# Optimization experiments

Hardware: AMD Instinct MI355X
Metric: run time of the kernel (lower is better)

The kernel has to match this reference:

```python
import jax, jax.numpy as jnp
import numpy as np

BN_EPS = 1e-5

def _haar_details(x):
    # pywt.dwt2(x, 'haar') details for even H, W.
    # Block [[p, q], [r, s]] with p = x[2i,2j], q = x[2i,2j+1], r = x[2i+1,2j], s = x[2i+1,2j+1].
    # cH ('da'): detail along rows, approx along cols; cV ('ad'); cD ('dd').
    B, C, H, W = x.shape
    xb = x.reshape(B, C, H // 2, 2, W // 2, 2)
    p = xb[:, :, :, 0, :, 0]
    q = xb[:, :, :, 0, :, 1]
    r = xb[:, :, :, 1, :, 0]
    s = xb[:, :, :, 1, :, 1]
    cH = (p + q - r - s) * 0.5
    cV = (p - q + r - s) * 0.5
    cD = (p - q - r + s) * 0.5
    return cH, cV, cD

def setup_inputs() -> dict:
    key = jax.random.key(0)
    k1, k2 = jax.random.split(key)
    B, C, H, W = 8, 256, 128, 128
    x = jax.random.normal(k1, (B, C, H, W), dtype=jnp.float32)
    conv_w = jax.random.normal(k2, (C, 4 * C), dtype=jnp.float32) * (1.0 / np.sqrt(4 * C))
    gamma = jnp.ones((C,), dtype=jnp.float32)
    beta = jnp.zeros((C,), dtype=jnp.float32)
    return {"x": x, "conv_w": conv_w, "gamma": gamma, "beta": beta}

def reference(x, conv_w, gamma, beta):
    B, C, H, W = x.shape
    # Original detaches the wavelet branch (CPU numpy path) -> stop_gradient.
    xs = jax.lax.stop_gradient(x)
    cH, cV, cD = _haar_details(xs)
    # Bilinear upsample to (H, W); jax.image.resize bilinear == torch align_corners=False.
    up = lambda t: jax.image.resize(t, (B, C, H, W), method="bilinear")
    enhanced = jnp.concatenate([x, up(cH), up(cV), up(cD)], axis=1)  # [B, 4C, H, W]
    # 1x1 conv, no bias.
    y = jnp.einsum("bchw,oc->bohw", enhanced, conv_w)  # [B, C, H, W]
    # BatchNorm2d, training-mode (batch statistics, biased variance).
    mean = jnp.mean(y, axis=(0, 2, 3), keepdims=True)
    var = jnp.mean((y - mean) ** 2, axis=(0, 2, 3), keepdims=True)
    y_hat = (y - mean) * jax.lax.rsqrt(var + BN_EPS)
    out = jax.nn.relu(y_hat * gamma[None, :, None, None] + beta[None, :, None, None])
    return out
```

## Files before the change

### kernel.cpp

```cpp
#include <hip/hip_runtime.h>
#include <hip/hip_bf16.h>

typedef __bf16 bf16;
typedef __bf16 bf16x4 __attribute__((ext_vector_type(4)));
typedef __bf16 bf16x8 __attribute__((ext_vector_type(8)));
typedef float  f32x4  __attribute__((ext_vector_type(4)));

__global__ __launch_bounds__(256) void prep_w(const float* __restrict__ w,
                                              bf16* __restrict__ wb) {
    const int o = blockIdx.x, c = threadIdx.x;
    const float* wr = w + o * 1024;
    const float w1 = wr[c], w2 = wr[256 + c], w3 = wr[512 + c], w4 = wr[768 + c];
    bf16* wo_ = wb + o * 1280;
    wo_[c]              = (bf16)w1;
    wo_[256 + 0*256 + c] = (bf16)(0.5f * ( w2 + w3 + w4));
    wo_[256 + 1*256 + c] = (bf16)(0.5f * ( w2 - w3 - w4));
    wo_[256 + 2*256 + c] = (bf16)(0.5f * (-w2 + w3 - w4));
    wo_[256 + 3*256 + c] = (bf16)(0.5f * (-w2 - w3 + w4));
}

__device__ __forceinline__ int tix(int row, int chunk, int lo) {
    int g = (row & 7) ^ ((row >> 2) & 7);
    return row * 256 + (((chunk ^ g) << 3) | lo);
}

__global__ __launch_bounds__(256, 2) void fused_x(const float* __restrict__ x,
                                                  const bf16* __restrict__ W,
                                                  bf16* __restrict__ z,
                                                  bf16* __restrict__ y1) {
    __shared__ bf16 tile[128 * 256];
    const int bid = blockIdx.x;
    const int half = bid & 1, j = (bid >> 1) & 63, b = bid >> 7;
    const int t = threadIdx.x;
    const int wave = t >> 6, lane = t & 63;
    const int quad = lane >> 4, l16 = lane & 15;
    const int wo = wave * 64;

    #pragma unroll
    for (int it = 0; it < 4; ++it) {
        const int a   = it * 256 + t;
        const int c8  = a >> 5;
        const int rem = a & 31;
        const int dlt = rem >> 4, w4 = rem & 15;
        const float* xp = x + (((size_t)b * 256 + c8 * 8) * 128 + (2*j + dlt)) * 128
                            + half * 64 + w4 * 4;
        float4 v[8];
        #pragma unroll
        for (int i = 0; i < 8; ++i)
            v[i] = *(const float4*)(xp + (size_t)i * 16384);
        #pragma unroll
        for (int e = 0; e < 4; ++e) {
            bf16x8 o8;
            #pragma unroll
            for (int i = 0; i < 8; ++i) o8[i] = (bf16)((&v[i].x)[e]);
            const int pos = dlt * 64 + w4 * 4 + e;
            *(bf16x8*)&tile[tix(pos, c8, 0)] = o8;
        }
    }

    bf16x8 wf_cur[4], wf_nxt[4];
    #pragma unroll
    for (int jj = 0; jj < 4; ++jj)
        wf_cur[jj] = *(const bf16x8*)(W +
            (size_t)(wo + jj * 16 + l16) * 1280 + quad * 8);

    __syncthreads();

    {
        f32x4 acc[8][4] = {};
        #pragma unroll
        for (int kk = 0; kk < 256; kk += 32) {
            if (kk < 224) {
                #pragma unroll
                for (int jj = 0; jj < 4; ++jj)
                    wf_nxt[jj] = *(const bf16x8*)(W +
                        (size_t)(wo + jj * 16 + l16) * 1280 + kk + 32 + quad * 8);
            } else {
                #pragma unroll
                for (int jj = 0; jj < 4; ++jj)
                    wf_nxt[jj] = *(const bf16x8*)(W +
                        (size_t)(wo + jj * 16 + l16) * 1280 + 256 + quad * 8);
            }
            const int kc0 = kk >> 3;
            #pragma unroll
            for (int i2 = 0; i2 < 8; ++i2) {
                const bf16x8 xf = *(const bf16x8*)&tile[tix(i2 * 16 + l16,
                                                            kc0 + quad, 0)];
                #pragma unroll
                for (int jj = 0; jj < 4; ++jj)
                    acc[i2][jj] = __builtin_amdgcn_mfma_f32_16x16x32_bf16(
                        xf, wf_cur[jj], acc[i2][jj], 0, 0, 0);
            }
            #pragma unroll
            for (int jj = 0; jj < 4; ++jj) wf_cur[jj] = wf_nxt[jj];
        }

        #pragma unroll
        for (int i2 = 0; i2 < 8; ++i2) {
            int p = i2 * 16 + quad * 4;
            int h = 2 * j + (p >> 6), wc = half * 64 + (p & 63);
            #pragma unroll
            for (int jj = 0; jj < 4; ++jj) {
                int o = wo + jj * 16 + l16;
                bf16x4 vv;
                #pragma unroll
                for (int r = 0; r < 4; ++r) vv[r] = (bf16)acc[i2][jj][r];
                *(bf16x4*)(y1 + ((size_t)b * 256 + o) * 16384 + h * 128 + wc) = vv;
            }
        }
    }

    f32x4 acc2[2][4] = {};
    #pragma unroll
    for (int kz = 0; kz < 1024; kz += 32) {
        if (kz < 992) {
            #pragma unroll
            for (int jj = 0; jj < 4; ++jj)
                wf_nxt[jj] = *(const bf16x8*)(W +
                    (size_t)(wo + jj * 16 + l16) * 1280 + 256 + kz + 32 + quad * 8);
        }
        const int tap = kz >> 8;
        const int dlt = tap >> 1, par = tap & 1;
        const int kc0 = (kz & 255) >> 3;
        bf16x8 af[2];
        #pragma unroll
        for (int mi = 0; mi < 2; ++mi)
            af[mi] = *(const bf16x8*)&tile[tix(dlt * 64 + 2 * (mi * 16 + l16) + par,
                                               kc0 + quad, 0)];
        #pragma unroll
        for (int mi = 0; mi < 2; ++mi)
            #pragma unroll
            for (int jj = 0; jj < 4; ++jj)
                acc2[mi][jj] = __builtin_amdgcn_mfma_f32_16x16x32_bf16(
                    af[mi], wf_cur[jj], acc2[mi][jj], 0, 0, 0);
        #pragma unroll
        for (int jj = 0; jj < 4; ++jj) wf_cur[jj] = wf_nxt[jj];
    }

    #pragma unroll
    for (int mi = 0; mi < 2; ++mi) {
        #pragma unroll
        for (int jj = 0; jj < 4; ++jj) {
            int o = wo + jj * 16 + l16;
            int cw = half * 32 + mi * 16 + quad * 4;
            bf16x4 vv;
            #pragma unroll
            for (int r = 0; r < 4; ++r) vv[r] = (bf16)acc2[mi][jj][r];
            *(bf16x4*)(z + ((size_t)b * 256 + o) * 4096 + j * 64 + cw) = vv;
        }
    }
}

__device__ __forceinline__ void load_zplane(const bf16* zp, float* zs, int t) {
    for (int i = 0; i < 2; ++i) {
        int idx = (i * 256 + t) * 8;
        int j = idx >> 6, k = idx & 63;
        bf16x8 v = *(const bf16x8*)(zp + idx);
        #pragma unroll
        for (int e = 0; e < 8; ++e) zs[j * 65 + k + e] = (float)v[e];
    }
}

__device__ __forceinline__ void up8(const float* zs, int base, float* u) {
    int h = base >> 7, w0 = base & 127;
    int j0 = h >> 1;
    int jn = (h & 1) ? min(j0 + 1, 63) : max(j0 - 1, 0);
    int K = w0 >> 1;
    float z0[6], z1[6];
    #pragma unroll
    for (int d = 0; d < 6; ++d) {
        int kc = min(max(K - 1 + d, 0), 63);
        z0[d] = zs[j0 * 65 + kc];
        z1[d] = zs[jn * 65 + kc];
    }
    #pragma unroll
    for (int e = 0; e < 8; ++e) {
        int a = (e >> 1) + 1;
        int bb = (e & 1) ? a + 1 : a - 1;
        u[e] = 0.5625f * z0[a] + 0.1875f * (z0[bb] + z1[a]) + 0.0625f * z1[bb];
    }
}

__global__ __launch_bounds__(256) void stats_k(const bf16* __restrict__ y1,
                                               const bf16* __restrict__ z,
                                               float* __restrict__ stats) {
    __shared__ float zs[64 * 65];
    __shared__ float red[8];
    const int bid = blockIdx.x;
    const int o = bid & 255, b = bid >> 8;
    const int t = threadIdx.x;
    const bf16* zp = z + ((size_t)b * 256 + o) * 4096;
    const bf16* yp = y1 + ((size_t)b * 256 + o) * 16384;
    load_zplane(zp, zs, t);
    __syncthreads();
    float s = 0.f, ss = 0.f;
    for (int i = 0; i < 8; ++i) {
        int base = (i * 256 + t) * 8;
        float u[8];
        up8(zs, base, u);
        bf16x8 yv = *(const bf16x8*)(yp + base);
        #pragma unroll
        for (int e = 0; e < 8; ++e) {
            float y = (float)yv[e] + u[e];
            s += y; ss += y * y;
        }
    }
    #pragma unroll
    for (int off = 32; off > 0; off >>= 1) {
        s += __shfl_down(s, off);
        ss += __shfl_down(ss, off);
    }
    if ((t & 63) == 0) { red[t >> 6] = s; red[4 + (t >> 6)] = ss; }
    __syncthreads();
    if (t == 0) {
        atomicAdd(&stats[o],       red[0] + red[1] + red[2] + red[3]);
        atomicAdd(&stats[256 + o], red[4] + red[5] + red[6] + red[7]);
    }
}

__global__ __launch_bounds__(256) void apply_k(const bf16* __restrict__ y1,
                                               const bf16* __restrict__ z,
                                               const float* __restrict__ stats,
                                               const float* __restrict__ gamma,
                                               const float* __restrict__ beta,
                                               float* __restrict__ out) {
    __shared__ float zs[64 * 65];
    const int bid = blockIdx.x;
    const int o = bid & 255, b = bid >> 8;
    const int t = threadIdx.x;
    const bf16* zp = z + ((size_t)b * 256 + o) * 4096;
    const bf16* yp = y1 + ((size_t)b * 256 + o) * 16384;
    float* op = out + ((size_t)b * 256 + o) * 16384;
    const float n = 131072.f;
    float mean = stats[o] / n;
    float var = stats[256 + o] / n - mean * mean;
    float sc = rsqrtf(var + 1e-5f) * gamma[o];
    float sh = beta[o] - mean * sc;
    load_zplane(zp, zs, t);
    __syncthreads();
    for (int i = 0; i < 8; ++i) {
        int base = (i * 256 + t) * 8;
        float u[8];
        up8(zs, base, u);
        bf16x8 yv = *(const bf16x8*)(yp + base);
        float4 o0, o1;
        o0.x = fmaxf(fmaf((float)yv[0] + u[0], sc, sh), 0.f);
        o0.y = fmaxf(fmaf((float)yv[1] + u[1], sc, sh), 0.f);
        o0.z = fmaxf(fmaf((float)yv[2] + u[2], sc, sh), 0.f);
        o0.w = fmaxf(fmaf((float)yv[3] + u[3], sc, sh), 0.f);
        o1.x = fmaxf(fmaf((float)yv[4] + u[4], sc, sh), 0.f);
        o1.y = fmaxf(fmaf((float)yv[5] + u[5], sc, sh), 0.f);
        o1.z = fmaxf(fmaf((float)yv[6] + u[6], sc, sh), 0.f);
        o1.w = fmaxf(fmaf((float)yv[7] + u[7], sc, sh), 0.f);
        *(float4*)(op + base) = o0;
        *(float4*)(op + base + 4) = o1;
    }
}

extern "C" void kernel_launch(void* const* d_in, const int* in_sizes, int n_in,
                              void* d_out, int out_size, void* d_ws, size_t ws_size,
                              hipStream_t stream) {
    const float* x      = (const float*)d_in[0];
    const float* conv_w = (const float*)d_in[1];
    const float* gamma  = (const float*)d_in[2];
    const float* beta   = (const float*)d_in[3];
    float* out = (float*)d_out;

    char* ws = (char*)d_ws;
    bf16*  Wbf   = (bf16*)ws;
    bf16*  z     = (bf16*)(ws + (1ll << 20));
    float* stats = (float*)(ws + (17ll << 20));
    bf16*  y1    = (bf16*)(ws + (17ll << 20) + (1ll << 16));

    hipMemsetAsync(stats, 0, 4096, stream);
    prep_w<<<256, 256, 0, stream>>>(conv_w, Wbf);
    fused_x<<<1024, 256, 0, stream>>>(x, Wbf, z, y1);
    stats_k<<<2048, 256, 0, stream>>>(y1, z, stats);
    apply_k<<<2048, 256, 0, stream>>>(y1, z, stats, gamma, beta, out);
}
```

Baseline: 353.6 us.

## Split fused GEMM across 8 waves and prefetch y loads in stats/apply

The fused x kernel now runs 512 threads per block, with each wave owning 32 output channels instead of 64. This halves the accumulators per wave and adds a two-deep weight prefetch in the z loop. In the stats and apply kernels, all eight y1 vectors are loaded before the barrier, and the z plane is stored as float4 with a 68-float row pitch. The goal is more latency hiding and memory parallelism, at the cost of more LDS reads of the x tile per output and higher register pressure in the elementwise kernels.

```diff
diff --git a/kernel.cpp b/kernel.cpp
--- a/kernel.cpp
+++ b/kernel.cpp
@@ -24,7 +24,7 @@
     return row * 256 + (((chunk ^ g) << 3) | lo);
 }
 
-__global__ __launch_bounds__(256, 2) void fused_x(const float* __restrict__ x,
+__global__ __launch_bounds__(512, 4) void fused_x(const float* __restrict__ x,
                                                   const bf16* __restrict__ W,
                                                   bf16* __restrict__ z,
                                                   bf16* __restrict__ y1) {
@@ -34,11 +34,11 @@
     const int t = threadIdx.x;
     const int wave = t >> 6, lane = t & 63;
     const int quad = lane >> 4, l16 = lane & 15;
-    const int wo = wave * 64;
-
-    #pragma unroll
-    for (int it = 0; it < 4; ++it) {
-        const int a   = it * 256 + t;
+    const int wo2 = wave * 32;
+
+    #pragma unroll
+    for (int it = 0; it < 2; ++it) {
+        const int a   = it * 512 + t;
         const int c8  = a >> 5;
         const int rem = a & 31;
         const int dlt = rem >> 4, w4 = rem & 15;
@@ -58,28 +58,28 @@
         }
     }
 
-    bf16x8 wf_cur[4], wf_nxt[4];
-    #pragma unroll
-    for (int jj = 0; jj < 4; ++jj)
+    bf16x8 wf_cur[2], wf_nxt[2];
+    #pragma unroll
+    for (int jj = 0; jj < 2; ++jj)
         wf_cur[jj] = *(const bf16x8*)(W +
-            (size_t)(wo + jj * 16 + l16) * 1280 + quad * 8);
+            (size_t)(wo2 + jj * 16 + l16) * 1280 + quad * 8);
 
     __syncthreads();
 
     {
-        f32x4 acc[8][4] = {};
+        f32x4 acc[8][2] = {};
         #pragma unroll
         for (int kk = 0; kk < 256; kk += 32) {
             if (kk < 224) {
                 #pragma unroll
-                for (int jj = 0; jj < 4; ++jj)
+                for (int jj = 0; jj < 2; ++jj)
                     wf_nxt[jj] = *(const bf16x8*)(W +
-                        (size_t)(wo + jj * 16 + l16) * 1280 + kk + 32 + quad * 8);
+                        (size_t)(wo2 + jj * 16 + l16) * 1280 + kk + 32 + quad * 8);
             } else {
                 #pragma unroll
-                for (int jj = 0; jj < 4; ++jj)
+                for (int jj = 0; jj < 2; ++jj)
                     wf_nxt[jj] = *(const bf16x8*)(W +
-                        (size_t)(wo + jj * 16 + l16) * 1280 + 256 + quad * 8);
+                        (size_t)(wo2 + jj * 16 + l16) * 1280 + 256 + quad * 8);
             }
             const int kc0 = kk >> 3;
             #pragma unroll
@@ -87,21 +87,26 @@
                 const bf16x8 xf = *(const bf16x8*)&tile[tix(i2 * 16 + l16,
                                                             kc0 + quad, 0)];
                 #pragma unroll
-                for (int jj = 0; jj < 4; ++jj)
+                for (int jj = 0; jj < 2; ++jj)
                     acc[i2][jj] = __builtin_amdgcn_mfma_f32_16x16x32_bf16(
                         xf, wf_cur[jj], acc[i2][jj], 0, 0, 0);
             }
             #pragma unroll
-            for (int jj = 0; jj < 4; ++jj) wf_cur[jj] = wf_nxt[jj];
-        }
+            for (int jj = 0; jj < 2; ++jj) wf_cur[jj] = wf_nxt[jj];
+        }
+
+        #pragma unroll
+        for (int jj = 0; jj < 2; ++jj)
+            wf_nxt[jj] = *(const bf16x8*)(W +
+                (size_t)(wo2 + jj * 16 + l16) * 1280 + 256 + 32 + quad * 8);
 
         #pragma unroll
         for (int i2 = 0; i2 < 8; ++i2) {
             int p = i2 * 16 + quad * 4;
             int h = 2 * j + (p >> 6), wc = half * 64 + (p & 63);
             #pragma unroll
-            for (int jj = 0; jj < 4; ++jj) {
-                int o = wo + jj * 16 + l16;
+            for (int jj = 0; jj < 2; ++jj) {
+                int o = wo2 + jj * 16 + l16;
                 bf16x4 vv;
                 #pragma unroll
                 for (int r = 0; r < 4; ++r) vv[r] = (bf16)acc[i2][jj][r];
@@ -110,14 +115,15 @@
         }
     }
 
-    f32x4 acc2[2][4] = {};
+    f32x4 acc2[2][2] = {};
     #pragma unroll
     for (int kz = 0; kz < 1024; kz += 32) {
-        if (kz < 992) {
-            #pragma unroll
-            for (int jj = 0; jj < 4; ++jj)
-                wf_nxt[jj] = *(const bf16x8*)(W +
-                    (size_t)(wo + jj * 16 + l16) * 1280 + 256 + kz + 32 + quad * 8);
+        bf16x8 wf_nx2[2];
+        if (kz < 960) {
+            #pragma unroll
+            for (int jj = 0; jj < 2; ++jj)
+                wf_nx2[jj] = *(const bf16x8*)(W +
+                    (size_t)(wo2 + jj * 16 + l16) * 1280 + 256 + kz + 64 + quad * 8);
         }
         const int tap = kz >> 8;
         const int dlt = tap >> 1, par = tap & 1;
@@ -130,18 +136,18 @@
         #pragma unroll
         for (int mi = 0; mi < 2; ++mi)
             #pragma unroll
-            for (int jj = 0; jj < 4; ++jj)
+            for (int jj = 0; jj < 2; ++jj)
                 acc2[mi][jj] = __builtin_amdgcn_mfma_f32_16x16x32_bf16(
                     af[mi], wf_cur[jj], acc2[mi][jj], 0, 0, 0);
         #pragma unroll
-        for (int jj = 0; jj < 4; ++jj) wf_cur[jj] = wf_nxt[jj];
+        for (int jj = 0; jj < 2; ++jj) { wf_cur[jj] = wf_nxt[jj]; wf_nxt[jj] = wf_nx2[jj]; }
     }
 
     #pragma unroll
     for (int mi = 0; mi < 2; ++mi) {
         #pragma unroll
-        for (int jj = 0; jj < 4; ++jj) {
-            int o = wo + jj * 16 + l16;
+        for (int jj = 0; jj < 2; ++jj) {
+            int o = wo2 + jj * 16 + l16;
             int cw = half * 32 + mi * 16 + quad * 4;
             bf16x4 vv;
             #pragma unroll
@@ -151,13 +157,19 @@
     }
 }
 
+#define ZS 68
+
 __device__ __forceinline__ void load_zplane(const bf16* zp, float* zs, int t) {
+    #pragma unroll
     for (int i = 0; i < 2; ++i) {
         int idx = (i * 256 + t) * 8;
         int j = idx >> 6, k = idx & 63;
         bf16x8 v = *(const bf16x8*)(zp + idx);
-        #pragma unroll
-        for (int e = 0; e < 8; ++e) zs[j * 65 + k + e] = (float)v[e];
+        float4 a, bq;
+        a.x  = (float)v[0]; a.y  = (float)v[1]; a.z  = (float)v[2]; a.w  = (float)v[3];
+        bq.x = (float)v[4]; bq.y = (float)v[5]; bq.z = (float)v[6]; bq.w = (float)v[7];
+        *(float4*)&zs[j * ZS + k]     = a;
+        *(float4*)&zs[j * ZS + k + 4] = bq;
     }
 }
 
@@ -166,12 +178,14 @@
     int j0 = h >> 1;
     int jn = (h & 1) ? min(j0 + 1, 63) : max(j0 - 1, 0);
     int K = w0 >> 1;
+    const float* r0 = zs + j0 * ZS;
+    const float* r1 = zs + jn * ZS;
     float z0[6], z1[6];
     #pragma unroll
     for (int d = 0; d < 6; ++d) {
         int kc = min(max(K - 1 + d, 0), 63);
-        z0[d] = zs[j0 * 65 + kc];
-        z1[d] = zs[jn * 65 + kc];
+        z0[d] = r0[kc];
+        z1[d] = r1[kc];
     }
     #pragma unroll
     for (int e = 0; e < 8; ++e) {
@@ -184,7 +198,7 @@
 __global__ __launch_bounds__(256) void stats_k(const bf16* __restrict__ y1,
                                                const bf16* __restrict__ z,
                                                float* __restrict__ stats) {
-    __shared__ float zs[64 * 65];
+    __shared__ float zs[64 * ZS];
     __shared__ float red[8];
     const int bid = blockIdx.x;
     const int o = bid & 255, b = bid >> 8;
@@ -192,16 +206,20 @@
     const bf16* zp = z + ((size_t)b * 256 + o) * 4096;
     const bf16* yp = y1 + ((size_t)b * 256 + o) * 16384;
     load_zplane(zp, zs, t);
+    bf16x8 yv[8];
+    #pragma unroll
+    for (int i = 0; i < 8; ++i)
+        yv[i] = *(const bf16x8*)(yp + (i * 256 + t) * 8);
     __syncthreads();
     float s = 0.f, ss = 0.f;
+    #pragma unroll
     for (int i = 0; i < 8; ++i) {
         int base = (i * 256 + t) * 8;
         float u[8];
         up8(zs, base, u);
-        bf16x8 yv = *(const bf16x8*)(yp + base);
         #pragma unroll
         for (int e = 0; e < 8; ++e) {
-            float y = (float)yv[e] + u[e];
+            float y = (float)yv[i][e] + u[e];
             s += y; ss += y * y;
         }
     }
@@ -224,7 +242,7 @@
                                                const float* __restrict__ gamma,
                                                const float* __restrict__ beta,
                                                float* __restrict__ out) {
-    __shared__ float zs[64 * 65];
+    __shared__ float zs[64 * ZS];
     const int bid = blockIdx.x;
     const int o = bid & 255, b = bid >> 8;
     const int t = threadIdx.x;
@@ -237,21 +255,25 @@
     float sc = rsqrtf(var + 1e-5f) * gamma[o];
     float sh = beta[o] - mean * sc;
     load_zplane(zp, zs, t);
+    bf16x8 yv[8];
+    #pragma unroll
+    for (int i = 0; i < 8; ++i)
+        yv[i] = *(const bf16x8*)(yp + (i * 256 + t) * 8);
     __syncthreads();
+    #pragma unroll
     for (int i = 0; i < 8; ++i) {
         int base = (i * 256 + t) * 8;
         float u[8];
         up8(zs, base, u);
-        bf16x8 yv = *(const bf16x8*)(yp + base);
         float4 o0, o1;
-        o0.x = fmaxf(fmaf((float)yv[0] + u[0], sc, sh), 0.f);
-        o0.y = fmaxf(fmaf((float)yv[1] + u[1], sc, sh), 0.f);
-        o0.z = fmaxf(fmaf((float)yv[2] + u[2], sc, sh), 0.f);
-        o0.w = fmaxf(fmaf((float)yv[3] + u[3], sc, sh), 0.f);
-        o1.x = fmaxf(fmaf((float)yv[4] + u[4], sc, sh), 0.f);
-        o1.y = fmaxf(fmaf((float)yv[5] + u[5], sc, sh), 0.f);
-        o1.z = fmaxf(fmaf((float)yv[6] + u[6], sc, sh), 0.f);
-        o1.w = fmaxf(fmaf((float)yv[7] + u[7], sc, sh), 0.f);
+        o0.x = fmaxf(fmaf((float)yv[i][0] + u[0], sc, sh), 0.f);
+        o0.y = fmaxf(fmaf((float)yv[i][1] + u[1], sc, sh), 0.f);
+        o0.z = fmaxf(fmaf((float)yv[i][2] + u[2], sc, sh), 0.f);
+        o0.w = fmaxf(fmaf((float)yv[i][3] + u[3], sc, sh), 0.f);
+        o1.x = fmaxf(fmaf((float)yv[i][4] + u[4], sc, sh), 0.f);
+        o1.y = fmaxf(fmaf((float)yv[i][5] + u[5], sc, sh), 0.f);
+        o1.z = fmaxf(fmaf((float)yv[i][6] + u[6], sc, sh), 0.f);
+        o1.w = fmaxf(fmaf((float)yv[i][7] + u[7], sc, sh), 0.f);
         *(float4*)(op + base) = o0;
         *(float4*)(op + base + 4) = o1;
     }
@@ -274,7 +296,7 @@
 
     hipMemsetAsync(stats, 0, 4096, stream);
     prep_w<<<256, 256, 0, stream>>>(conv_w, Wbf);
-    fused_x<<<1024, 256, 0, stream>>>(x, Wbf, z, y1);
+    fused_x<<<1024, 512, 0, stream>>>(x, Wbf, z, y1);
     stats_k<<<2048, 256, 0, stream>>>(y1, z, stats);
     apply_k<<<2048, 256, 0, stream>>>(y1, z, stats, gamma, beta, out);
 }
```

After: 347.1 us. No clear change (-1.8%).
